# Kernel optimization log

Hardware: AMD Instinct MI355X
Metric: run time of the kernel (lower is better)

## Reference

```python
import jax, jax.numpy as jnp
import numpy as np

B = 100          # batch_size -> dist matrix is [2B, 2B]
G = 2            # pairs
REG = 0.1
H = W = 256
EPS = 1e-08


def computemask(b, g):
    # Faithful numpy port of the torch computemask (pure python, constants).
    Mask, labels = [], []
    mtxsize = 2 * b
    for j in range(mtxsize):
        i = j
        x = [i - i % g - i // b * b,
             i + 1 - i % g - i // b * b,
             i - i % g - i // b * b + b,
             i + 1 - i % g - i // b * b + b]
        x.remove(j)
        for xi in x:
            xx = x.copy()
            indexs = list(range(mtxsize))
            indexs.remove(j)
            xx.remove(xi)
            for r in xx:
                indexs.remove(r)
            labels.append(indexs.index(xi))
            Mask.append(indexs)
    return np.asarray(Mask, np.int32), np.asarray(labels, np.int32)


def setup_inputs() -> dict:
    key = jax.random.key(0)
    x = jax.random.normal(key, (2 * B, 1, H, W), dtype=jnp.float32)
    m, l = computemask(B, G)              # [6B, 2B-3], [6B]
    return {"x": x, "masks": jnp.asarray(m), "labels": jnp.asarray(l)}


def _euclidean_distance_matrix(x):
    xf = x.reshape(x.shape[0], -1)                      # [N, H*W]
    dot = xf @ xf.T                                     # [N, N] Gram GEMM
    sq = jnp.diagonal(dot)
    d = sq[None, :] - 2.0 * dot + sq[:, None]
    d = jnp.maximum(d, 0.0)
    mask = (d == 0.0).astype(x.dtype)
    d = jnp.sqrt(d + mask * EPS) * (1.0 - mask)
    return d


def _calc_psd(xs):
    dft = jnp.fft.fft2(xs)                              # [N, H, W] complex
    avgpsd = jnp.mean((dft * jnp.conj(dft)).real, axis=0)  # [H, W]
    return jnp.mean(jnp.log(avgpsd)) - jnp.log(jnp.mean(avgpsd))


def reference(x, masks, labels):
    xs = jnp.squeeze(x)                                 # [2B, H, W]
    dist = _euclidean_distance_matrix(xs)               # [2B, 2B]
    # create_pairs: logits[m] = dist[m // 3][masks[m]]  -> [6B, 2B-3]
    rows = jnp.arange(masks.shape[0]) // 3
    logits = dist[rows[:, None], masks]
    logp = jax.nn.log_softmax(logits, axis=-1)
    ce = -jnp.mean(logp[jnp.arange(labels.shape[0]), labels])
    return ce - REG * _calc_psd(xs)
```

## Files before the change

### kernel.cpp

```cpp
#include <hip/hip_runtime.h>
#include <hip/hip_bf16.h>
#include <math.h>


#define NIMG 200
#define NROW 256
#define NCOL 256
#define NPIX 65536
#define TSTR 132
#define ISTR 264
#define XSTR 273
#define NCH  50
#define IPC  4
#define GNK  64
#define GKC  1024

typedef float2 c2;
typedef short bf16x8 __attribute__((ext_vector_type(8)));
typedef unsigned short u16x8 __attribute__((ext_vector_type(8)));
typedef float f32x4  __attribute__((ext_vector_type(4)));

__device__ __forceinline__ unsigned short f2b(float f) {
    union { float f; unsigned int u; } c; c.f = f;
    unsigned int r = (c.u + 0x7FFFu + ((c.u >> 16) & 1u)) >> 16;
    return (unsigned short)r;
}
__device__ __forceinline__ float b2f(unsigned short b) {
    union { unsigned int u; float f; } c; c.u = ((unsigned int)b) << 16;
    return c.f;
}

__device__ __forceinline__ c2 cmul(c2 a, c2 b) {
    return make_float2(a.x*b.x - a.y*b.y, a.x*b.y + a.y*b.x);
}
__device__ __forceinline__ c2 cadd(c2 a, c2 b){ return make_float2(a.x+b.x, a.y+b.y); }
__device__ __forceinline__ c2 csub(c2 a, c2 b){ return make_float2(a.x-b.x, a.y-b.y); }
__device__ __forceinline__ c2 mulmi(c2 a){ return make_float2(a.y, -a.x); }

__device__ __forceinline__ void fft4(c2& a, c2& b, c2& c, c2& d) {
    c2 t0 = cadd(a,c), t1 = csub(a,c), t2 = cadd(b,d), t3 = csub(b,d);
    a = cadd(t0,t2);
    c = csub(t0,t2);
    c2 mt3 = mulmi(t3);
    b = cadd(t1, mt3);
    d = csub(t1, mt3);
}

__device__ __forceinline__ void fft16(c2 x[16]) {
    #pragma unroll
    for (int j=0;j<4;j++) fft4(x[j], x[4+j], x[8+j], x[12+j]);
    const c2 W1 = make_float2( 0.9238795325112867f,-0.3826834323650898f);
    const c2 W2 = make_float2( 0.7071067811865476f,-0.7071067811865476f);
    const c2 W3 = make_float2( 0.3826834323650898f,-0.9238795325112867f);
    const c2 W6 = make_float2(-0.7071067811865476f,-0.7071067811865476f);
    const c2 W9 = make_float2(-0.9238795325112867f, 0.3826834323650898f);
    x[5]=cmul(x[5],W1);   x[6]=cmul(x[6],W2);   x[7]=cmul(x[7],W3);
    x[9]=cmul(x[9],W2);   x[10]=mulmi(x[10]);   x[11]=cmul(x[11],W6);
    x[13]=cmul(x[13],W3); x[14]=cmul(x[14],W6); x[15]=cmul(x[15],W9);
    #pragma unroll
    for (int k1=0;k1<4;k1++) fft4(x[4*k1], x[4*k1+1], x[4*k1+2], x[4*k1+3]);
}
#define R4(q) ((((q)&3)<<2)|((q)>>2))

__global__ __launch_bounds__(512) void k_gemm(const unsigned short* __restrict__ Xb,
                                              float* __restrict__ Pg) {
    __shared__ unsigned short As[128*64];
    __shared__ unsigned short Bs[128*64];
    int p  = blockIdx.x;
    int kc = blockIdx.y;
    int ti = p >> 1, tj = (p + 1) >> 1;
    bool diag = (ti == tj);
    int i0 = ti << 7, j0 = tj << 7;
    int tid = threadIdx.x;
    int wid = tid >> 6, lane = tid & 63;
    int wr = wid >> 2, wc = wid & 3;

    f32x4 acc[4][2];
    #pragma unroll
    for (int a=0;a<4;a++)
        #pragma unroll
        for (int b=0;b<2;b++) acc[a][b] = (f32x4){0.f,0.f,0.f,0.f};

    int srow = tid >> 2, g0 = (tid & 3) * 2;
    int gia = i0 + srow; if (gia > 199) gia = 199;
    int gjb = j0 + srow; if (gjb > 199) gjb = 199;
    const u16x8* Ap = (const u16x8*)(Xb + (size_t)gia*NPIX + kc*GKC);
    const u16x8* Bp = (const u16x8*)(Xb + (size_t)gjb*NPIX + kc*GKC);
    int e0 = (srow*128 + g0*16) ^ ((srow & 7) << 4);
    int e1 = (srow*128 + (g0+1)*16) ^ ((srow & 7) << 4);

    int swz = (lane & 7) << 3;
    int acol0 = (lane >> 4) << 3;

    u16x8 ca0 = Ap[g0], ca1 = Ap[g0+1];
    u16x8 cb0, cb1;
    if (!diag) { cb0 = Bp[g0]; cb1 = Bp[g0+1]; }

    for (int st = 0; st < GKC/64; ++st) {
        __syncthreads();
        *(u16x8*)((char*)As + e0) = ca0;
        *(u16x8*)((char*)As + e1) = ca1;
        if (!diag) {
            *(u16x8*)((char*)Bs + e0) = cb0;
            *(u16x8*)((char*)Bs + e1) = cb1;
        }
        if (st < GKC/64 - 1) {
            ca0 = Ap[(st+1)*8 + g0]; ca1 = Ap[(st+1)*8 + g0+1];
            if (!diag) { cb0 = Bp[(st+1)*8 + g0]; cb1 = Bp[(st+1)*8 + g0+1]; }
        }
        __syncthreads();
        const unsigned short* Bb = diag ? As : Bs;
        #pragma unroll
        for (int ks=0; ks<2; ++ks) {
            int col = (ks*32 + acol0) ^ swz;
            bf16x8 af[4], bfv[2];
            #pragma unroll
            for (int mf=0; mf<4; ++mf) {
                int r = wr*64 + mf*16 + (lane & 15);
                af[mf] = *(const bf16x8*)(&As[r*64 + col]);
            }
            #pragma unroll
            for (int nf=0; nf<2; ++nf) {
                int r = wc*32 + nf*16 + (lane & 15);
                bfv[nf] = *(const bf16x8*)(&Bb[r*64 + col]);
            }
            #pragma unroll
            for (int mf=0; mf<4; ++mf)
                #pragma unroll
                for (int nf=0; nf<2; ++nf)
                    acc[mf][nf] = __builtin_amdgcn_mfma_f32_16x16x32_bf16(af[mf], bfv[nf], acc[mf][nf], 0, 0, 0);
        }
    }
    float* P = Pg + ((size_t)p*GNK + kc)*16384;
    #pragma unroll
    for (int mf=0; mf<4; ++mf) {
        int m0 = wr*64 + mf*16 + ((lane >> 4) << 2);
        #pragma unroll
        for (int nf=0; nf<2; ++nf) {
            int n = wc*32 + nf*16 + (lane & 15);
            #pragma unroll
            for (int r2=0; r2<4; ++r2)
                P[(size_t)(m0+r2)*128 + n] = acc[mf][nf][r2];
        }
    }
}

__global__ __launch_bounds__(256) void k_gredu(const float* __restrict__ Pg,
                                               float* __restrict__ dotm) {
    int idx = blockIdx.x*256 + threadIdx.x;
    if (idx >= 200*200) return;
    int i = idx / 200, j = idx - i*200;
    int ti = i >> 7, tj = j >> 7;
    int p, li, lj;
    if (ti <= tj) { p = ti + tj; li = i - (ti << 7); lj = j - (tj << 7); }
    else          { p = 1;       li = j;             lj = i - 128; }
    const float* base = Pg + (size_t)p*GNK*16384 + (size_t)li*128 + lj;
    float s0=0.f, s1=0.f, s2=0.f, s3=0.f;
    #pragma unroll 4
    for (int kc=0; kc<GNK; kc+=4) {
        s0 += base[(size_t)(kc  )*16384];
        s1 += base[(size_t)(kc+1)*16384];
        s2 += base[(size_t)(kc+2)*16384];
        s3 += base[(size_t)(kc+3)*16384];
    }
    dotm[(size_t)i*200 + j] = (s0+s1) + (s2+s3);
}

__global__ __launch_bounds__(256) void k_rowfft(const float* __restrict__ x,
                                                ushort2* __restrict__ T,
                                                unsigned short* __restrict__ Xb) {
    __shared__ __align__(16) char ldsraw[16*XSTR*4];
    float*   inpF = (float*)ldsraw;
    ushort2* tb   = (ushort2*)ldsraw;
    int tid = threadIdx.x;
    int img = blockIdx.y;
    int rg  = blockIdx.x;
    int g = tid >> 4, t = tid & 15;
    int row = rg*16 + g;

    const float4* xr = (const float4*)(x + (size_t)img*NPIX + (size_t)row*NCOL + t*16);
    float4 v0 = xr[0], v1 = xr[1], v2 = xr[2], v3 = xr[3];
    u16x8 h0, h1;
    h0[0]=f2b(v0.x); h0[1]=f2b(v0.y); h0[2]=f2b(v0.z); h0[3]=f2b(v0.w);
    h0[4]=f2b(v1.x); h0[5]=f2b(v1.y); h0[6]=f2b(v1.z); h0[7]=f2b(v1.w);
    h1[0]=f2b(v2.x); h1[1]=f2b(v2.y); h1[2]=f2b(v2.z); h1[3]=f2b(v2.w);
    h1[4]=f2b(v3.x); h1[5]=f2b(v3.y); h1[6]=f2b(v3.z); h1[7]=f2b(v3.w);
    u16x8* Xo = (u16x8*)(Xb + (size_t)img*NPIX + (size_t)row*NCOL + t*16);
    Xo[0] = h0; Xo[1] = h1;
    float* ip = inpF + g*ISTR + t*16;
    *(float4*)(ip)    = v0;
    *(float4*)(ip+4)  = v1;
    *(float4*)(ip+8)  = v2;
    *(float4*)(ip+12) = v3;
    __syncthreads();

    c2 y[16];
    #pragma unroll
    for (int n1=0;n1<16;n1++) y[n1] = make_float2(inpF[g*ISTR + 16*n1 + t], 0.f);
    fft16(y);
    {
        float sv, cv;
        sincosf(-0.024543692606170259f * (float)t, &sv, &cv);
        c2 Wb = make_float2(cv, sv);
        c2 cur = Wb;
        #pragma unroll
        for (int r=1;r<16;r++) { y[R4(r)] = cmul(y[R4(r)], cur); cur = cmul(cur, Wb); }
    }
    __syncthreads();
    #pragma unroll
    for (int r=0;r<16;r++) {
        c2 v = y[R4(r)];
        tb[g*XSTR + t*17 + r] = make_ushort2(f2b(v.x), f2b(v.y));
    }
    __syncthreads();

    c2 w[16];
    #pragma unroll
    for (int n2=0;n2<16;n2++) {
        ushort2 u = tb[g*XSTR + n2*17 + t];
        w[n2] = make_float2(b2f(u.x), b2f(u.y));
    }
    fft16(w);
    ushort2* To = T + ((size_t)img*NROW + row)*TSTR;
    #pragma unroll
    for (int q=0;q<8;q++) {
        c2 v = w[R4(q)];
        To[q*16 + t] = make_ushort2(f2b(v.x), f2b(v.y));
    }
    if (t == 0) { c2 v = w[R4(8)]; To[128] = make_ushort2(f2b(v.x), f2b(v.y)); }
}

__global__ __launch_bounds__(256) void k_colfft(const ushort2* __restrict__ T,
                                                float* __restrict__ Ppart) {
    __shared__ ushort2 sb[16][XSTR];
    int tid = threadIdx.x;
    int c0 = blockIdx.x * 16;
    int ic = blockIdx.y;
    int g = tid >> 4, t = tid & 15;
    int cc = tid & 15, rb = tid >> 4;
    int cl = c0 + cc; if (cl > 128) cl = 128;
    c2 Wb;
    {
        float sv, cv;
        sincosf(-0.024543692606170259f * (float)t, &sv, &cv);
        Wb = make_float2(cv, sv);
    }
    float pacc[16];
    #pragma unroll
    for (int q=0;q<16;q++) pacc[q] = 0.f;

    for (int li=0; li<IPC; ++li) {
        int img = ic*IPC + li;
        __syncthreads();
        const ushort2* Tb = T + (size_t)img*NROW*TSTR;
        #pragma unroll
        for (int j=0;j<16;j++) {
            int r = rb*16 + j;
            sb[cc][r] = Tb[(size_t)r*TSTR + cl];
        }
        __syncthreads();
        c2 y[16];
        #pragma unroll
        for (int n1=0;n1<16;n1++) {
            ushort2 u = sb[g][16*n1 + t];
            y[n1] = make_float2(b2f(u.x), b2f(u.y));
        }
        fft16(y);
        {
            c2 cur = Wb;
            #pragma unroll
            for (int r=1;r<16;r++) { y[R4(r)] = cmul(y[R4(r)], cur); cur = cmul(cur, Wb); }
        }
        __syncthreads();
        #pragma unroll
        for (int r=0;r<16;r++) {
            c2 v = y[R4(r)];
            sb[g][t*17 + r] = make_ushort2(f2b(v.x), f2b(v.y));
        }
        __syncthreads();
        c2 w[16];
        #pragma unroll
        for (int n2=0;n2<16;n2++) {
            ushort2 u = sb[g][n2*17 + t];
            w[n2] = make_float2(b2f(u.x), b2f(u.y));
        }
        fft16(w);
        #pragma unroll
        for (int q=0;q<16;q++) { c2 v = w[R4(q)]; pacc[q] += v.x*v.x + v.y*v.y; }
    }
    int c = c0 + g;
    if (c <= 128) {
        float* PP = Ppart + ((size_t)ic*132 + c)*256;
        #pragma unroll
        for (int q=0;q<16;q++) PP[q*16 + t] = pacc[q];
    }
}

__global__ __launch_bounds__(256) void k_tail(const float* __restrict__ Ppart,
                                              const float* __restrict__ dotm,
                                              const int* __restrict__ masks,
                                              const int* __restrict__ labels,
                                              float* __restrict__ cep,
                                              float2* __restrict__ Pred) {
    int bid = blockIdx.x, tid = threadIdx.x;
    if (bid < 129) {
        int c = bid;
        float s = 0.f;
        for (int ic=0; ic<NCH; ++ic) s += Ppart[((size_t)ic*132 + c)*256 + tid];
        float v = s * (1.0f/200.0f);
        float w = (c == 0 || c == 128) ? 1.f : 2.f;
        float sl = w * logf(v);
        float ss = w * v;
        __shared__ float r2[2][4];
        int wv = tid>>6, ln = tid&63;
        #pragma unroll
        for (int off=32; off>=1; off>>=1) {
            sl += __shfl_xor(sl, off);
            ss += __shfl_xor(ss, off);
        }
        if (ln == 0) { r2[0][wv] = sl; r2[1][wv] = ss; }
        __syncthreads();
        if (tid == 0)
            Pred[c] = make_float2(r2[0][0]+r2[0][1]+r2[0][2]+r2[0][3],
                                  r2[1][0]+r2[1][1]+r2[1][2]+r2[1][3]);
    } else {
        int m = (bid - 129)*4 + (tid >> 6);
        if (m >= 600) return;
        int lane = tid & 63;
        int i = m / 3;
        float sqi = dotm[(size_t)i*200 + i];
        int lbl = labels[m];
        float lg[4];
        float vmax = -1e30f, lsel = 0.f;
        #pragma unroll
        for (int k=0;k<4;k++) {
            int c = lane + 64*k;
            float v = -1e30f;
            if (c < 197) {
                int j = masks[(size_t)m*197 + c];
                float d = sqi + dotm[(size_t)j*200 + j] - 2.f*dotm[(size_t)i*200 + j];
                d = fmaxf(d, 0.f);
                v = (d == 0.f) ? 0.f : sqrtf(d);
                if (c == lbl) lsel = v;
            }
            lg[k] = v;
            vmax = fmaxf(vmax, v);
        }
        #pragma unroll
        for (int off=32; off>=1; off>>=1) vmax = fmaxf(vmax, __shfl_xor(vmax, off));
        float se = 0.f;
        #pragma unroll
        for (int k=0;k<4;k++) if (lg[k] > -1e29f) se += expf(lg[k] - vmax);
        #pragma unroll
        for (int off=32; off>=1; off>>=1) { se += __shfl_xor(se, off); lsel += __shfl_xor(lsel, off); }
        if (lane == 0) cep[m] = lsel - (vmax + logf(se));
    }
}

__global__ __launch_bounds__(256) void k_final(const float2* __restrict__ Pred,
                                               const float* __restrict__ cep,
                                               float* __restrict__ out) {
    int tid = threadIdx.x;
    float sl = 0.f, ss = 0.f, sce = 0.f;
    if (tid < 129) { float2 p = Pred[tid]; sl = p.x; ss = p.y; }
    for (int m = tid; m < 600; m += 256) sce += cep[m];
    __shared__ float r3[3][4];
    int wv = tid>>6, ln = tid&63;
    #pragma unroll
    for (int off=32; off>=1; off>>=1) {
        sl  += __shfl_xor(sl, off);
        ss  += __shfl_xor(ss, off);
        sce += __shfl_xor(sce, off);
    }
    if (ln == 0) { r3[0][wv]=sl; r3[1][wv]=ss; r3[2][wv]=sce; }
    __syncthreads();
    if (tid == 0) {
        float SL = r3[0][0]+r3[0][1]+r3[0][2]+r3[0][3];
        float SS = r3[1][0]+r3[1][1]+r3[1][2]+r3[1][3];
        float CE = r3[2][0]+r3[2][1]+r3[2][2]+r3[2][3];
        float ce  = -CE / 600.f;
        float psd = SL * (1.f/65536.f) - logf(SS * (1.f/65536.f));
        out[0] = ce - 0.1f * psd;
    }
}

extern "C" void kernel_launch(void* const* d_in, const int* in_sizes, int n_in,
                              void* d_out, int out_size, void* d_ws, size_t ws_size,
                              hipStream_t stream) {
    const float* x      = (const float*)d_in[0];
    const int*   masks  = (const int*)d_in[1];
    const int*   labels = (const int*)d_in[2];
    float* out = (float*)d_out;
    char* ws = (char*)d_ws;

    const size_t OFF_DOT = 0;
    const size_t OFF_CE  = 160256;
    const size_t OFF_PR  = 162688;
    const size_t OFF_PP  = 163840;
    const size_t OFF_T   = 6922240;
    const size_t OFF_XB  = 33955840;
    const size_t OFF_PG  = 60170240;
    const size_t NEED    = 72753152;
    if (ws_size < NEED) return;

    float*          dotm = (float*)(ws + OFF_DOT);
    float*          cep  = (float*)(ws + OFF_CE);
    float2*         Pr   = (float2*)(ws + OFF_PR);
    float*          Pp   = (float*)(ws + OFF_PP);
    ushort2*        T    = (ushort2*)(ws + OFF_T);
    unsigned short* Xb   = (unsigned short*)(ws + OFF_XB);
    float*          Pg   = (float*)(ws + OFF_PG);

    k_rowfft<<<dim3(16,200), dim3(256), 0, stream>>>(x, T, Xb);
    k_gemm  <<<dim3(3, GNK), dim3(512), 0, stream>>>(Xb, Pg);
    k_gredu <<<dim3(157),    dim3(256), 0, stream>>>(Pg, dotm);
    k_colfft<<<dim3(9,NCH),  dim3(256), 0, stream>>>(T, Pp);
    k_tail  <<<dim3(279),    dim3(256), 0, stream>>>(Pp, dotm, masks, labels, cep, Pr);
    k_final <<<dim3(1),      dim3(256), 0, stream>>>(Pr, cep, out);
}
```

Measured before the change: 76.07 us.

## Double the K-split count and prefetch two stages ahead in Gram GEMM

New measurement: 89.12 us. +17.1%, slower.

```diff
diff --git a/kernel.cpp b/kernel.cpp
--- a/kernel.cpp
+++ b/kernel.cpp
@@ -12,8 +12,9 @@
 #define XSTR 273
 #define NCH  50
 #define IPC  4
-#define GNK  64
-#define GKC  1024
+#define GNK  128
+#define GKC  512
+#define NSTEP 8
 
 typedef float2 c2;
 typedef short bf16x8 __attribute__((ext_vector_type(8)));
@@ -92,23 +93,7 @@
     int swz = (lane & 7) << 3;
     int acol0 = (lane >> 4) << 3;
 
-    u16x8 ca0 = Ap[g0], ca1 = Ap[g0+1];
-    u16x8 cb0, cb1;
-    if (!diag) { cb0 = Bp[g0]; cb1 = Bp[g0+1]; }
-
-    for (int st = 0; st < GKC/64; ++st) {
-        __syncthreads();
-        *(u16x8*)((char*)As + e0) = ca0;
-        *(u16x8*)((char*)As + e1) = ca1;
-        if (!diag) {
-            *(u16x8*)((char*)Bs + e0) = cb0;
-            *(u16x8*)((char*)Bs + e1) = cb1;
-        }
-        if (st < GKC/64 - 1) {
-            ca0 = Ap[(st+1)*8 + g0]; ca1 = Ap[(st+1)*8 + g0+1];
-            if (!diag) { cb0 = Bp[(st+1)*8 + g0]; cb1 = Bp[(st+1)*8 + g0+1]; }
-        }
-        __syncthreads();
+    auto do_mfma = [&]() {
         const unsigned short* Bb = diag ? As : Bs;
         #pragma unroll
         for (int ks=0; ks<2; ++ks) {
@@ -130,7 +115,46 @@
                 for (int nf=0; nf<2; ++nf)
                     acc[mf][nf] = __builtin_amdgcn_mfma_f32_16x16x32_bf16(af[mf], bfv[nf], acc[mf][nf], 0, 0, 0);
         }
-    }
+    };
+
+    u16x8 a0_0 = Ap[g0],     a0_1 = Ap[g0+1];
+    u16x8 a1_0 = Ap[8 + g0], a1_1 = Ap[8 + g0+1];
+    u16x8 b0_0, b0_1, b1_0, b1_1;
+    if (!diag) {
+        b0_0 = Bp[g0];     b0_1 = Bp[g0+1];
+        b1_0 = Bp[8 + g0]; b1_1 = Bp[8 + g0+1];
+    }
+
+    #pragma unroll 1
+    for (int k = 0; k < NSTEP; k += 2) {
+        __syncthreads();
+        *(u16x8*)((char*)As + e0) = a0_0;
+        *(u16x8*)((char*)As + e1) = a0_1;
+        if (!diag) {
+            *(u16x8*)((char*)Bs + e0) = b0_0;
+            *(u16x8*)((char*)Bs + e1) = b0_1;
+        }
+        if (k + 2 < NSTEP) {
+            a0_0 = Ap[(k+2)*8 + g0]; a0_1 = Ap[(k+2)*8 + g0+1];
+            if (!diag) { b0_0 = Bp[(k+2)*8 + g0]; b0_1 = Bp[(k+2)*8 + g0+1]; }
+        }
+        __syncthreads();
+        do_mfma();
+        __syncthreads();
+        *(u16x8*)((char*)As + e0) = a1_0;
+        *(u16x8*)((char*)As + e1) = a1_1;
+        if (!diag) {
+            *(u16x8*)((char*)Bs + e0) = b1_0;
+            *(u16x8*)((char*)Bs + e1) = b1_1;
+        }
+        if (k + 3 < NSTEP) {
+            a1_0 = Ap[(k+3)*8 + g0]; a1_1 = Ap[(k+3)*8 + g0+1];
+            if (!diag) { b1_0 = Bp[(k+3)*8 + g0]; b1_1 = Bp[(k+3)*8 + g0+1]; }
+        }
+        __syncthreads();
+        do_mfma();
+    }
+
     float* P = Pg + ((size_t)p*GNK + kc)*16384;
     #pragma unroll
     for (int mf=0; mf<4; ++mf) {
@@ -400,7 +424,7 @@
     const size_t OFF_T   = 6922240;
     const size_t OFF_XB  = 33955840;
     const size_t OFF_PG  = 60170240;
-    const size_t NEED    = 72753152;
+    const size_t NEED    = 85336064;
     if (ws_size < NEED) return;
 
     float*          dotm = (float*)(ws + OFF_DOT);
```

## Double-buffer GEMM tiles with direct global-to-LDS async loads

Applied to the files above, without the earlier changes.

Result: slower. 80.45 us (+5.7%).

```diff
diff --git a/kernel.cpp b/kernel.cpp
--- a/kernel.cpp
+++ b/kernel.cpp
@@ -14,11 +14,17 @@
 #define IPC  4
 #define GNK  64
 #define GKC  1024
+#define NST  16
 
 typedef float2 c2;
 typedef short bf16x8 __attribute__((ext_vector_type(8)));
 typedef unsigned short u16x8 __attribute__((ext_vector_type(8)));
 typedef float f32x4  __attribute__((ext_vector_type(4)));
+
+#define GLDS16(gsrc, ldst) \
+    __builtin_amdgcn_global_load_lds( \
+        (const __attribute__((address_space(1))) void*)(gsrc), \
+        (__attribute__((address_space(3))) void*)(ldst), 16, 0, 0)
 
 __device__ __forceinline__ unsigned short f2b(float f) {
     union { float f; unsigned int u; } c; c.f = f;
@@ -64,16 +70,16 @@
 
 __global__ __launch_bounds__(512) void k_gemm(const unsigned short* __restrict__ Xb,
                                               float* __restrict__ Pg) {
-    __shared__ unsigned short As[128*64];
-    __shared__ unsigned short Bs[128*64];
+    __shared__ unsigned short As[2][128*64];
+    __shared__ unsigned short Bs[2][128*64];
     int p  = blockIdx.x;
     int kc = blockIdx.y;
     int ti = p >> 1, tj = (p + 1) >> 1;
     bool diag = (ti == tj);
     int i0 = ti << 7, j0 = tj << 7;
     int tid = threadIdx.x;
-    int wid = tid >> 6, lane = tid & 63;
-    int wr = wid >> 2, wc = wid & 3;
+    int wv = tid >> 6, lane = tid & 63;
+    int wr = wv >> 2, wc = wv & 3;
 
     f32x4 acc[4][2];
     #pragma unroll
@@ -81,35 +87,49 @@
         #pragma unroll
         for (int b=0;b<2;b++) acc[a][b] = (f32x4){0.f,0.f,0.f,0.f};
 
-    int srow = tid >> 2, g0 = (tid & 3) * 2;
-    int gia = i0 + srow; if (gia > 199) gia = 199;
-    int gjb = j0 + srow; if (gjb > 199) gjb = 199;
-    const u16x8* Ap = (const u16x8*)(Xb + (size_t)gia*NPIX + kc*GKC);
-    const u16x8* Bp = (const u16x8*)(Xb + (size_t)gjb*NPIX + kc*GKC);
-    int e0 = (srow*128 + g0*16) ^ ((srow & 7) << 4);
-    int e1 = (srow*128 + (g0+1)*16) ^ ((srow & 7) << 4);
+    int row0 = wv*16 + (lane >> 3);
+    int row1 = row0 + 8;
+    int gs0 = (lane & 7) ^ (row0 & 7);
+    int gs1 = (lane & 7) ^ (row1 & 7);
+    int ra0 = i0 + row0; if (ra0 > 199) ra0 = 199;
+    int ra1 = i0 + row1; if (ra1 > 199) ra1 = 199;
+    int rb0 = j0 + row0; if (rb0 > 199) rb0 = 199;
+    int rb1 = j0 + row1; if (rb1 > 199) rb1 = 199;
+    const unsigned short* gA0 = Xb + (size_t)ra0*NPIX + kc*GKC + gs0*8;
+    const unsigned short* gA1 = Xb + (size_t)ra1*NPIX + kc*GKC + gs1*8;
+    const unsigned short* gB0 = Xb + (size_t)rb0*NPIX + kc*GKC + gs0*8;
+    const unsigned short* gB1 = Xb + (size_t)rb1*NPIX + kc*GKC + gs1*8;
+    int ldsOff0 = (wv*16    )*64;
+    int ldsOff1 = (wv*16 + 8)*64;
 
     int swz = (lane & 7) << 3;
     int acol0 = (lane >> 4) << 3;
 
-    u16x8 ca0 = Ap[g0], ca1 = Ap[g0+1];
-    u16x8 cb0, cb1;
-    if (!diag) { cb0 = Bp[g0]; cb1 = Bp[g0+1]; }
-
-    for (int st = 0; st < GKC/64; ++st) {
-        __syncthreads();
-        *(u16x8*)((char*)As + e0) = ca0;
-        *(u16x8*)((char*)As + e1) = ca1;
+    auto stage = [&](int buf, int st) {
+        GLDS16(gA0 + st*64, &As[buf][ldsOff0]);
+        GLDS16(gA1 + st*64, &As[buf][ldsOff1]);
         if (!diag) {
-            *(u16x8*)((char*)Bs + e0) = cb0;
-            *(u16x8*)((char*)Bs + e1) = cb1;
-        }
-        if (st < GKC/64 - 1) {
-            ca0 = Ap[(st+1)*8 + g0]; ca1 = Ap[(st+1)*8 + g0+1];
-            if (!diag) { cb0 = Bp[(st+1)*8 + g0]; cb1 = Bp[(st+1)*8 + g0+1]; }
-        }
-        __syncthreads();
-        const unsigned short* Bb = diag ? As : Bs;
+            GLDS16(gB0 + st*64, &Bs[buf][ldsOff0]);
+            GLDS16(gB1 + st*64, &Bs[buf][ldsOff1]);
+        }
+    };
+
+    stage(0, 0);
+    stage(1, 1);
+
+    #pragma unroll 1
+    for (int st = 0; st < NST; ++st) {
+        int P = st & 1;
+        if (st < NST - 1) {
+            if (diag) asm volatile("s_waitcnt vmcnt(2)" ::: "memory");
+            else      asm volatile("s_waitcnt vmcnt(4)" ::: "memory");
+        } else {
+            asm volatile("s_waitcnt vmcnt(0)" ::: "memory");
+        }
+        __builtin_amdgcn_s_barrier();
+        __builtin_amdgcn_sched_barrier(0);
+        const unsigned short* Ab = &As[P][0];
+        const unsigned short* Bb = diag ? Ab : &Bs[P][0];
         #pragma unroll
         for (int ks=0; ks<2; ++ks) {
             int col = (ks*32 + acol0) ^ swz;
@@ -117,7 +137,7 @@
             #pragma unroll
             for (int mf=0; mf<4; ++mf) {
                 int r = wr*64 + mf*16 + (lane & 15);
-                af[mf] = *(const bf16x8*)(&As[r*64 + col]);
+                af[mf] = *(const bf16x8*)(&Ab[r*64 + col]);
             }
             #pragma unroll
             for (int nf=0; nf<2; ++nf) {
@@ -130,8 +150,13 @@
                 for (int nf=0; nf<2; ++nf)
                     acc[mf][nf] = __builtin_amdgcn_mfma_f32_16x16x32_bf16(af[mf], bfv[nf], acc[mf][nf], 0, 0, 0);
         }
-    }
-    float* P = Pg + ((size_t)p*GNK + kc)*16384;
+        __builtin_amdgcn_sched_barrier(0);
+        __builtin_amdgcn_s_barrier();
+        __builtin_amdgcn_sched_barrier(0);
+        if (st + 2 < NST) stage(P, st + 2);
+    }
+
+    float* P_ = Pg + ((size_t)p*GNK + kc)*16384;
     #pragma unroll
     for (int mf=0; mf<4; ++mf) {
         int m0 = wr*64 + mf*16 + ((lane >> 4) << 2);
@@ -140,7 +165,7 @@
             int n = wc*32 + nf*16 + (lane & 15);
             #pragma unroll
             for (int r2=0; r2<4; ++r2)
-                P[(size_t)(m0+r2)*128 + n] = acc[mf][nf][r2];
+                P_[(size_t)(m0+r2)*128 + n] = acc[mf][nf][r2];
         }
     }
 }
```

## Merge Gram GEMM and column FFT into one heterogeneous launch

Applied to the files above, without the earlier changes.

Result: faster. 73.74 us (-3.1%).

```diff
diff --git a/kernel.cpp b/kernel.cpp
--- a/kernel.cpp
+++ b/kernel.cpp
@@ -14,6 +14,7 @@
 #define IPC  4
 #define GNK  64
 #define GKC  1024
+#define CLDS 17472
 
 typedef float2 c2;
 typedef short bf16x8 __attribute__((ext_vector_type(8)));
@@ -62,85 +63,157 @@
 }
 #define R4(q) ((((q)&3)<<2)|((q)>>2))
 
-__global__ __launch_bounds__(512) void k_gemm(const unsigned short* __restrict__ Xb,
-                                              float* __restrict__ Pg) {
-    __shared__ unsigned short As[128*64];
-    __shared__ unsigned short Bs[128*64];
-    int p  = blockIdx.x;
-    int kc = blockIdx.y;
-    int ti = p >> 1, tj = (p + 1) >> 1;
-    bool diag = (ti == tj);
-    int i0 = ti << 7, j0 = tj << 7;
+__global__ __launch_bounds__(512) void k_gc(const unsigned short* __restrict__ Xb,
+                                            float* __restrict__ Pg,
+                                            const ushort2* __restrict__ T,
+                                            float* __restrict__ Ppart) {
+    __shared__ __align__(16) char smem[2*CLDS];
+    int bid = blockIdx.x;
     int tid = threadIdx.x;
-    int wid = tid >> 6, lane = tid & 63;
-    int wr = wid >> 2, wc = wid & 3;
-
-    f32x4 acc[4][2];
-    #pragma unroll
-    for (int a=0;a<4;a++)
-        #pragma unroll
-        for (int b=0;b<2;b++) acc[a][b] = (f32x4){0.f,0.f,0.f,0.f};
-
-    int srow = tid >> 2, g0 = (tid & 3) * 2;
-    int gia = i0 + srow; if (gia > 199) gia = 199;
-    int gjb = j0 + srow; if (gjb > 199) gjb = 199;
-    const u16x8* Ap = (const u16x8*)(Xb + (size_t)gia*NPIX + kc*GKC);
-    const u16x8* Bp = (const u16x8*)(Xb + (size_t)gjb*NPIX + kc*GKC);
-    int e0 = (srow*128 + g0*16) ^ ((srow & 7) << 4);
-    int e1 = (srow*128 + (g0+1)*16) ^ ((srow & 7) << 4);
-
-    int swz = (lane & 7) << 3;
-    int acol0 = (lane >> 4) << 3;
-
-    u16x8 ca0 = Ap[g0], ca1 = Ap[g0+1];
-    u16x8 cb0, cb1;
-    if (!diag) { cb0 = Bp[g0]; cb1 = Bp[g0+1]; }
-
-    for (int st = 0; st < GKC/64; ++st) {
-        __syncthreads();
-        *(u16x8*)((char*)As + e0) = ca0;
-        *(u16x8*)((char*)As + e1) = ca1;
-        if (!diag) {
-            *(u16x8*)((char*)Bs + e0) = cb0;
-            *(u16x8*)((char*)Bs + e1) = cb1;
-        }
-        if (st < GKC/64 - 1) {
-            ca0 = Ap[(st+1)*8 + g0]; ca1 = Ap[(st+1)*8 + g0+1];
-            if (!diag) { cb0 = Bp[(st+1)*8 + g0]; cb1 = Bp[(st+1)*8 + g0+1]; }
-        }
-        __syncthreads();
-        const unsigned short* Bb = diag ? As : Bs;
-        #pragma unroll
-        for (int ks=0; ks<2; ++ks) {
-            int col = (ks*32 + acol0) ^ swz;
-            bf16x8 af[4], bfv[2];
-            #pragma unroll
-            for (int mf=0; mf<4; ++mf) {
-                int r = wr*64 + mf*16 + (lane & 15);
-                af[mf] = *(const bf16x8*)(&As[r*64 + col]);
-            }
+
+    if (bid < 192) {
+        unsigned short* As = (unsigned short*)smem;
+        unsigned short* Bs = (unsigned short*)(smem + 16384);
+        int p  = bid >> 6;
+        int kc = bid & 63;
+        int ti = p >> 1, tj = (p + 1) >> 1;
+        bool diag = (ti == tj);
+        int i0 = ti << 7, j0 = tj << 7;
+        int wid = tid >> 6, lane = tid & 63;
+        int wr = wid >> 2, wc = wid & 3;
+
+        f32x4 acc[4][2];
+        #pragma unroll
+        for (int a=0;a<4;a++)
+            #pragma unroll
+            for (int b=0;b<2;b++) acc[a][b] = (f32x4){0.f,0.f,0.f,0.f};
+
+        int srow = tid >> 2, g0 = (tid & 3) * 2;
+        int gia = i0 + srow; if (gia > 199) gia = 199;
+        int gjb = j0 + srow; if (gjb > 199) gjb = 199;
+        const u16x8* Ap = (const u16x8*)(Xb + (size_t)gia*NPIX + kc*GKC);
+        const u16x8* Bp = (const u16x8*)(Xb + (size_t)gjb*NPIX + kc*GKC);
+        int e0 = (srow*128 + g0*16) ^ ((srow & 7) << 4);
+        int e1 = (srow*128 + (g0+1)*16) ^ ((srow & 7) << 4);
+
+        int swz = (lane & 7) << 3;
+        int acol0 = (lane >> 4) << 3;
+
+        u16x8 ca0 = Ap[g0], ca1 = Ap[g0+1];
+        u16x8 cb0, cb1;
+        if (!diag) { cb0 = Bp[g0]; cb1 = Bp[g0+1]; }
+
+        for (int st = 0; st < GKC/64; ++st) {
+            __syncthreads();
+            *(u16x8*)(As ? (char*)As + e0 : 0) = ca0;
+            *(u16x8*)((char*)As + e1) = ca1;
+            if (!diag) {
+                *(u16x8*)((char*)Bs + e0) = cb0;
+                *(u16x8*)((char*)Bs + e1) = cb1;
+            }
+            if (st < GKC/64 - 1) {
+                ca0 = Ap[(st+1)*8 + g0]; ca1 = Ap[(st+1)*8 + g0+1];
+                if (!diag) { cb0 = Bp[(st+1)*8 + g0]; cb1 = Bp[(st+1)*8 + g0+1]; }
+            }
+            __syncthreads();
+            const unsigned short* Bb = diag ? As : Bs;
+            #pragma unroll
+            for (int ks=0; ks<2; ++ks) {
+                int col = (ks*32 + acol0) ^ swz;
+                bf16x8 af[4], bfv[2];
+                #pragma unroll
+                for (int mf=0; mf<4; ++mf) {
+                    int r = wr*64 + mf*16 + (lane & 15);
+                    af[mf] = *(const bf16x8*)(&As[r*64 + col]);
+                }
+                #pragma unroll
+                for (int nf=0; nf<2; ++nf) {
+                    int r = wc*32 + nf*16 + (lane & 15);
+                    bfv[nf] = *(const bf16x8*)(&Bb[r*64 + col]);
+                }
+                #pragma unroll
+                for (int mf=0; mf<4; ++mf)
+                    #pragma unroll
+                    for (int nf=0; nf<2; ++nf)
+                        acc[mf][nf] = __builtin_amdgcn_mfma_f32_16x16x32_bf16(af[mf], bfv[nf], acc[mf][nf], 0, 0, 0);
+            }
+        }
+        float* P = Pg + ((size_t)p*GNK + kc)*16384;
+        #pragma unroll
+        for (int mf=0; mf<4; ++mf) {
+            int m0 = wr*64 + mf*16 + ((lane >> 4) << 2);
             #pragma unroll
             for (int nf=0; nf<2; ++nf) {
-                int r = wc*32 + nf*16 + (lane & 15);
-                bfv[nf] = *(const bf16x8*)(&Bb[r*64 + col]);
-            }
-            #pragma unroll
-            for (int mf=0; mf<4; ++mf)
+                int n = wc*32 + nf*16 + (lane & 15);
                 #pragma unroll
-                for (int nf=0; nf<2; ++nf)
-                    acc[mf][nf] = __builtin_amdgcn_mfma_f32_16x16x32_bf16(af[mf], bfv[nf], acc[mf][nf], 0, 0, 0);
-        }
-    }
-    float* P = Pg + ((size_t)p*GNK + kc)*16384;
-    #pragma unroll
-    for (int mf=0; mf<4; ++mf) {
-        int m0 = wr*64 + mf*16 + ((lane >> 4) << 2);
-        #pragma unroll
-        for (int nf=0; nf<2; ++nf) {
-            int n = wc*32 + nf*16 + (lane & 15);
-            #pragma unroll
-            for (int r2=0; r2<4; ++r2)
-                P[(size_t)(m0+r2)*128 + n] = acc[mf][nf][r2];
+                for (int r2=0; r2<4; ++r2)
+                    P[(size_t)(m0+r2)*128 + n] = acc[mf][nf][r2];
+            }
+        }
+    } else {
+        int team = tid >> 8;
+        int t256 = tid & 255;
+        ushort2* sb = (ushort2*)(smem + team*CLDS);
+        int gteam = (bid - 192)*2 + team;
+        int cgi = gteam % 9, ic = gteam / 9;
+        int c0 = cgi * 16;
+        int g = t256 >> 4, t = t256 & 15;
+        int cc = t256 & 15, rb = t256 >> 4;
+        int cl = c0 + cc; if (cl > 128) cl = 128;
+        c2 Wb;
+        {
+            float sv, cv;
+            sincosf(-0.024543692606170259f * (float)t, &sv, &cv);
+            Wb = make_float2(cv, sv);
+        }
+        float pacc[16];
+        #pragma unroll
+        for (int q=0;q<16;q++) pacc[q] = 0.f;
+
+        for (int li=0; li<IPC; ++li) {
+            int img = ic*IPC + li;
+            __syncthreads();
+            const ushort2* Tb = T + (size_t)img*NROW*TSTR;
+            #pragma unroll
+            for (int j=0;j<16;j++) {
+                int r = rb*16 + j;
+                sb[cc*XSTR + r] = Tb[(size_t)r*TSTR + cl];
+            }
+            __syncthreads();
+            c2 y[16];
+            #pragma unroll
+            for (int n1=0;n1<16;n1++) {
+                ushort2 u = sb[g*XSTR + 16*n1 + t];
+                y[n1] = make_float2(b2f(u.x), b2f(u.y));
+            }
+            fft16(y);
+            {
+                c2 cur = Wb;
+                #pragma unroll
+                for (int r=1;r<16;r++) { y[R4(r)] = cmul(y[R4(r)], cur); cur = cmul(cur, Wb); }
+            }
+            __syncthreads();
+            #pragma unroll
+            for (int r=0;r<16;r++) {
+                c2 v = y[R4(r)];
+                sb[g*XSTR + t*17 + r] = make_ushort2(f2b(v.x), f2b(v.y));
+            }
+            __syncthreads();
+            c2 w[16];
+            #pragma unroll
+            for (int n2=0;n2<16;n2++) {
+                ushort2 u = sb[g*XSTR + n2*17 + t];
+                w[n2] = make_float2(b2f(u.x), b2f(u.y));
+            }
+            fft16(w);
+            #pragma unroll
+            for (int q=0;q<16;q++) { c2 v = w[R4(q)]; pacc[q] += v.x*v.x + v.y*v.y; }
+        }
+        int c = c0 + g;
+        if (c <= 128) {
+            float* PP = Ppart + ((size_t)ic*132 + c)*256;
+            #pragma unroll
+            for (int q=0;q<16;q++) PP[q*16 + t] = pacc[q];
         }
     }
 }
@@ -230,72 +303,6 @@
     if (t == 0) { c2 v = w[R4(8)]; To[128] = make_ushort2(f2b(v.x), f2b(v.y)); }
 }
 
-__global__ __launch_bounds__(256) void k_colfft(const ushort2* __restrict__ T,
-                                                float* __restrict__ Ppart) {
-    __shared__ ushort2 sb[16][XSTR];
-    int tid = threadIdx.x;
-    int c0 = blockIdx.x * 16;
-    int ic = blockIdx.y;
-    int g = tid >> 4, t = tid & 15;
-    int cc = tid & 15, rb = tid >> 4;
-    int cl = c0 + cc; if (cl > 128) cl = 128;
-    c2 Wb;
-    {
-        float sv, cv;
-        sincosf(-0.024543692606170259f * (float)t, &sv, &cv);
-        Wb = make_float2(cv, sv);
-    }
-    float pacc[16];
-    #pragma unroll
-    for (int q=0;q<16;q++) pacc[q] = 0.f;
-
-    for (int li=0; li<IPC; ++li) {
-        int img = ic*IPC + li;
-        __syncthreads();
-        const ushort2* Tb = T + (size_t)img*NROW*TSTR;
-        #pragma unroll
-        for (int j=0;j<16;j++) {
-            int r = rb*16 + j;
-            sb[cc][r] = Tb[(size_t)r*TSTR + cl];
-        }
-        __syncthreads();
-        c2 y[16];
-        #pragma unroll
-        for (int n1=0;n1<16;n1++) {
-            ushort2 u = sb[g][16*n1 + t];
-            y[n1] = make_float2(b2f(u.x), b2f(u.y));
-        }
-        fft16(y);
-        {
-            c2 cur = Wb;
-            #pragma unroll
-            for (int r=1;r<16;r++) { y[R4(r)] = cmul(y[R4(r)], cur); cur = cmul(cur, Wb); }
-        }
-        __syncthreads();
-        #pragma unroll
-        for (int r=0;r<16;r++) {
-            c2 v = y[R4(r)];
-            sb[g][t*17 + r] = make_ushort2(f2b(v.x), f2b(v.y));
-        }
-        __syncthreads();
-        c2 w[16];
-        #pragma unroll
-        for (int n2=0;n2<16;n2++) {
-            ushort2 u = sb[g][n2*17 + t];
-            w[n2] = make_float2(b2f(u.x), b2f(u.y));
-        }
-        fft16(w);
-        #pragma unroll
-        for (int q=0;q<16;q++) { c2 v = w[R4(q)]; pacc[q] += v.x*v.x + v.y*v.y; }
-    }
-    int c = c0 + g;
-    if (c <= 128) {
-        float* PP = Ppart + ((size_t)ic*132 + c)*256;
-        #pragma unroll
-        for (int q=0;q<16;q++) PP[q*16 + t] = pacc[q];
-    }
-}
-
 __global__ __launch_bounds__(256) void k_tail(const float* __restrict__ Ppart,
                                               const float* __restrict__ dotm,
                                               const int* __restrict__ masks,
@@ -412,9 +419,8 @@
     float*          Pg   = (float*)(ws + OFF_PG);
 
     k_rowfft<<<dim3(16,200), dim3(256), 0, stream>>>(x, T, Xb);
-    k_gemm  <<<dim3(3, GNK), dim3(512), 0, stream>>>(Xb, Pg);
+    k_gc    <<<dim3(417),    dim3(512), 0, stream>>>(Xb, Pg, T, Pp);
     k_gredu <<<dim3(157),    dim3(256), 0, stream>>>(Pg, dotm);
-    k_colfft<<<dim3(9,NCH),  dim3(256), 0, stream>>>(T, Pp);
     k_tail  <<<dim3(279),    dim3(256), 0, stream>>>(Pp, dotm, masks, labels, cep, Pr);
     k_final <<<dim3(1),      dim3(256), 0, stream>>>(Pr, cep, out);
 }
```
